# Performance work log

Measured on AMD Instinct MI355X. Metric: run time of the kernel, lower is better.

## Reference

```python
import jax, jax.numpy as jnp
import numpy as np


def ste_sign(x):
    # Forward: q(x) = +1 if x >= 0 else -1.
    # Backward: clipped straight-through estimator (identity on |x| <= 1).
    clipped = jnp.clip(x, -1.0, 1.0)
    binary = jnp.where(x >= 0, 1.0, -1.0).astype(x.dtype)
    return clipped + jax.lax.stop_gradient(binary - clipped)


BATCH = 16384
IN_FEATURES = 4096
UNITS = 512


def setup_inputs() -> dict:
    key = jax.random.key(0)
    kx, kw = jax.random.split(key)
    x = jax.random.normal(kx, (BATCH, IN_FEATURES), dtype=jnp.float32)
    # Latent full-precision kernel (kept in [-1,1]-ish range like a constrained BNN kernel)
    W = jax.random.normal(kw, (IN_FEATURES, UNITS), dtype=jnp.float32) * 0.5
    b = jnp.zeros((UNITS,), dtype=jnp.float32)
    return {"x": x, "W": W, "b": b}


def reference(x, W, b):
    # QuantizedDense: binarize inputs and kernel to +/-1, then standard dense matmul.
    xq = ste_sign(x)                # [B, F]
    Wq = ste_sign(W)                # [F, U]
    return jnp.dot(xq, Wq) + b      # [B, U]
```

## Files before the change

kernel.cpp:

```cpp
#include <hip/hip_runtime.h>
#include <stdint.h>


#define BATCH  16384
#define INF    4096
#define UNITS  512
#define KW     128
#define KW64   64
#define ROWSB  32
#define KC     8
#define NCH    16
#define SWW    12

__global__ __launch_bounds__(256) void pack_w_kernel(const float* __restrict__ W,
                                                     unsigned long long* __restrict__ Wp) {
    int t  = blockIdx.x * 256 + threadIdx.x;
    int u  = t & 511;
    int cj = t >> 9;
    int j  = cj & 3;
    int c  = cj >> 2;
    const float* base = W + (size_t)(c * 256 + j) * UNITS + u;
    unsigned long long m = 0;
    #pragma unroll 16
    for (int i = 0; i < 64; ++i) {
        float v = base[(size_t)(4 * i) * UNITS];
        m |= (unsigned long long)(v < 0.f) << i;
    }
    Wp[(size_t)u * KW64 + cj] = m;
}

__global__ __launch_bounds__(512) void fused_kernel(const float* __restrict__ x,
                                                    const uint32_t* __restrict__ Wp,
                                                    const float* __restrict__ bias,
                                                    float* __restrict__ C) {
    __shared__ __attribute__((aligned(16))) uint32_t sW[2][UNITS][SWW];
    const int t = threadIdx.x;
    const int w = t >> 6;
    const int l = t & 63;
    const int row0 = blockIdx.x * ROWSB;
    const float4* xf4 = reinterpret_cast<const float4*>(x);
    const int wrow = t >> 1;
    const int wcol = (t & 1) * 4;

    uint32_t acc[4][4] = {};
    unsigned long long xb[4][4];

    {
        uint4 wA = *reinterpret_cast<const uint4*>(Wp + (size_t)wrow * KW + wcol);
        uint4 wB = *reinterpret_cast<const uint4*>(Wp + ((size_t)wrow + 256) * KW + wcol);
        #pragma unroll
        for (int i = 0; i < 4; ++i) {
            float4 v = xf4[((size_t)(row0 + w * 4 + i) << 10) + l];
            xb[i][0] = __ballot(v.x < 0.f);
            xb[i][1] = __ballot(v.y < 0.f);
            xb[i][2] = __ballot(v.z < 0.f);
            xb[i][3] = __ballot(v.w < 0.f);
        }
        *reinterpret_cast<uint4*>(&sW[0][wrow][wcol]) = wA;
        *reinterpret_cast<uint4*>(&sW[0][wrow + 256][wcol]) = wB;
        __syncthreads();
    }

    for (int c = 0; c < NCH; ++c) {
        const int cb = c & 1, nb = cb ^ 1;
        const bool pf = (c + 1 < NCH);
        uint4 wA, wB;
        float4 xr[4];

        if (pf) {
            const uint32_t* wsrc = Wp + (c + 1) * KC;
            wA = *reinterpret_cast<const uint4*>(wsrc + (size_t)wrow * KW + wcol);
            wB = *reinterpret_cast<const uint4*>(wsrc + ((size_t)wrow + 256) * KW + wcol);
            #pragma unroll
            for (int i = 0; i < 4; ++i)
                xr[i] = xf4[((size_t)(row0 + w * 4 + i) << 10) + (size_t)(c + 1) * 64 + l];
        }

        #pragma unroll
        for (int j2 = 0; j2 < 4; ++j2) {
            const int u0 = l + 128 * j2;
            uint4 w0a = *reinterpret_cast<const uint4*>(&sW[cb][u0][0]);
            uint4 w0b = *reinterpret_cast<const uint4*>(&sW[cb][u0][4]);
            uint4 w1a = *reinterpret_cast<const uint4*>(&sW[cb][u0 + 64][0]);
            uint4 w1b = *reinterpret_cast<const uint4*>(&sW[cb][u0 + 64][4]);
            #pragma unroll
            for (int i = 0; i < 4; ++i) {
                uint32_t x0 = (uint32_t)xb[i][0], x1 = (uint32_t)(xb[i][0] >> 32);
                uint32_t x2 = (uint32_t)xb[i][1], x3 = (uint32_t)(xb[i][1] >> 32);
                uint32_t x4 = (uint32_t)xb[i][2], x5 = (uint32_t)(xb[i][2] >> 32);
                uint32_t x6 = (uint32_t)xb[i][3], x7 = (uint32_t)(xb[i][3] >> 32);
                uint32_t c0 = __popc(x0 ^ w0a.x) + __popc(x1 ^ w0a.y)
                            + __popc(x2 ^ w0a.z) + __popc(x3 ^ w0a.w)
                            + __popc(x4 ^ w0b.x) + __popc(x5 ^ w0b.y)
                            + __popc(x6 ^ w0b.z) + __popc(x7 ^ w0b.w);
                uint32_t c1 = __popc(x0 ^ w1a.x) + __popc(x1 ^ w1a.y)
                            + __popc(x2 ^ w1a.z) + __popc(x3 ^ w1a.w)
                            + __popc(x4 ^ w1b.x) + __popc(x5 ^ w1b.y)
                            + __popc(x6 ^ w1b.z) + __popc(x7 ^ w1b.w);
                acc[i][j2] += c0 + (c1 << 16);
            }
        }

        if (pf) {
            *reinterpret_cast<uint4*>(&sW[nb][wrow][wcol]) = wA;
            *reinterpret_cast<uint4*>(&sW[nb][wrow + 256][wcol]) = wB;
            #pragma unroll
            for (int i = 0; i < 4; ++i) {
                xb[i][0] = __ballot(xr[i].x < 0.f);
                xb[i][1] = __ballot(xr[i].y < 0.f);
                xb[i][2] = __ballot(xr[i].z < 0.f);
                xb[i][3] = __ballot(xr[i].w < 0.f);
            }
        }
        __syncthreads();
    }

    #pragma unroll
    for (int j2 = 0; j2 < 4; ++j2) {
        const int u0 = l + 128 * j2, u1 = u0 + 64;
        const float bv0 = bias[u0], bv1 = bias[u1];
        #pragma unroll
        for (int i = 0; i < 4; ++i) {
            size_t r = (size_t)(row0 + w * 4 + i) * UNITS;
            uint32_t pk = acc[i][j2];
            C[r + u0] = (float)(INF - 2 * (int)(pk & 0xFFFFu)) + bv0;
            C[r + u1] = (float)(INF - 2 * (int)(pk >> 16)) + bv1;
        }
    }
}

extern "C" void kernel_launch(void* const* d_in, const int* in_sizes, int n_in,
                              void* d_out, int out_size, void* d_ws, size_t ws_size,
                              hipStream_t stream) {
    const float* x = (const float*)d_in[0];
    const float* W = (const float*)d_in[1];
    const float* b = (const float*)d_in[2];
    float* out = (float*)d_out;

    unsigned long long* Wp = (unsigned long long*)d_ws;

    pack_w_kernel<<<32768 / 256, 256, 0, stream>>>(W, Wp);
    fused_kernel<<<BATCH / ROWSB, 512, 0, stream>>>(
        x, (const uint32_t*)Wp, b, out);
}
```

Before: 99.59 us.

## Stream packed weights from global into registers, dropping the shared-memory staging

The packed weight layout is changed so each lane can load uint4 fragments directly from global memory (L2-resident). The fused kernel drops the double-buffered shared-memory tile and the per-chunk __syncthreads, and uses 256-thread blocks where each wave handles 4 rows independently. Weight prefetch is split into two half-chunks that interleave with the popcount compute. This removes LDS traffic and block barriers, but raises register pressure and sends many redundant weight loads through the cache hierarchy.

```diff
diff --git a/kernel.cpp b/kernel.cpp
--- a/kernel.cpp
+++ b/kernel.cpp
@@ -6,14 +6,10 @@
 #define INF    4096
 #define UNITS  512
 #define KW     128
-#define KW64   64
-#define ROWSB  32
-#define KC     8
 #define NCH    16
-#define SWW    12
 
 __global__ __launch_bounds__(256) void pack_w_kernel(const float* __restrict__ W,
-                                                     unsigned long long* __restrict__ Wp) {
+                                                     uint32_t* __restrict__ Wp2) {
     int t  = blockIdx.x * 256 + threadIdx.x;
     int u  = t & 511;
     int cj = t >> 9;
@@ -26,84 +22,89 @@
         float v = base[(size_t)(4 * i) * UNITS];
         m |= (unsigned long long)(v < 0.f) << i;
     }
-    Wp[(size_t)u * KW64 + cj] = m;
+    uint32_t* dst = Wp2 + ((size_t)(c * 2 + (j >> 1)) * 512 + u) * 4 + 2 * (j & 1);
+    *reinterpret_cast<uint2*>(dst) = make_uint2((uint32_t)m, (uint32_t)(m >> 32));
 }
 
-__global__ __launch_bounds__(512) void fused_kernel(const float* __restrict__ x,
-                                                    const uint32_t* __restrict__ Wp,
-                                                    const float* __restrict__ bias,
-                                                    float* __restrict__ C) {
-    __shared__ __attribute__((aligned(16))) uint32_t sW[2][UNITS][SWW];
-    const int t = threadIdx.x;
-    const int w = t >> 6;
-    const int l = t & 63;
-    const int row0 = blockIdx.x * ROWSB;
+__global__ __launch_bounds__(256, 4) void fused_kernel(const float* __restrict__ x,
+                                                       const uint32_t* __restrict__ Wp2,
+                                                       const float* __restrict__ bias,
+                                                       float* __restrict__ C) {
+    const int t  = threadIdx.x;
+    const int l  = t & 63;
+    const int gw = (blockIdx.x * 256 + t) >> 6;
+    const int row0 = gw * 4;
     const float4* xf4 = reinterpret_cast<const float4*>(x);
-    const int wrow = t >> 1;
-    const int wcol = (t & 1) * 4;
+    const uint4*  Wq  = reinterpret_cast<const uint4*>(Wp2);
 
     uint32_t acc[4][4] = {};
     unsigned long long xb[4][4];
+    float4 xr[4];
+    uint4  wvA[8], wvB[8];
 
-    {
-        uint4 wA = *reinterpret_cast<const uint4*>(Wp + (size_t)wrow * KW + wcol);
-        uint4 wB = *reinterpret_cast<const uint4*>(Wp + ((size_t)wrow + 256) * KW + wcol);
-        #pragma unroll
-        for (int i = 0; i < 4; ++i) {
-            float4 v = xf4[((size_t)(row0 + w * 4 + i) << 10) + l];
-            xb[i][0] = __ballot(v.x < 0.f);
-            xb[i][1] = __ballot(v.y < 0.f);
-            xb[i][2] = __ballot(v.z < 0.f);
-            xb[i][3] = __ballot(v.w < 0.f);
-        }
-        *reinterpret_cast<uint4*>(&sW[0][wrow][wcol]) = wA;
-        *reinterpret_cast<uint4*>(&sW[0][wrow + 256][wcol]) = wB;
-        __syncthreads();
+    #pragma unroll
+    for (int i = 0; i < 4; ++i)
+        xr[i] = xf4[((size_t)(row0 + i) << 10) + l];
+    #pragma unroll
+    for (int jj = 0; jj < 8; ++jj)
+        wvA[jj] = Wq[(size_t)(jj * 64 + l)];
+    #pragma unroll
+    for (int jj = 0; jj < 8; ++jj)
+        wvB[jj] = Wq[(size_t)512 + jj * 64 + l];
+    #pragma unroll
+    for (int i = 0; i < 4; ++i) {
+        xb[i][0] = __ballot(xr[i].x < 0.f);
+        xb[i][1] = __ballot(xr[i].y < 0.f);
+        xb[i][2] = __ballot(xr[i].z < 0.f);
+        xb[i][3] = __ballot(xr[i].w < 0.f);
     }
 
+    #pragma unroll 1
     for (int c = 0; c < NCH; ++c) {
-        const int cb = c & 1, nb = cb ^ 1;
         const bool pf = (c + 1 < NCH);
-        uint4 wA, wB;
-        float4 xr[4];
 
         if (pf) {
-            const uint32_t* wsrc = Wp + (c + 1) * KC;
-            wA = *reinterpret_cast<const uint4*>(wsrc + (size_t)wrow * KW + wcol);
-            wB = *reinterpret_cast<const uint4*>(wsrc + ((size_t)wrow + 256) * KW + wcol);
             #pragma unroll
             for (int i = 0; i < 4; ++i)
-                xr[i] = xf4[((size_t)(row0 + w * 4 + i) << 10) + (size_t)(c + 1) * 64 + l];
+                xr[i] = xf4[((size_t)(row0 + i) << 10) + (size_t)(c + 1) * 64 + l];
         }
 
         #pragma unroll
-        for (int j2 = 0; j2 < 4; ++j2) {
-            const int u0 = l + 128 * j2;
-            uint4 w0a = *reinterpret_cast<const uint4*>(&sW[cb][u0][0]);
-            uint4 w0b = *reinterpret_cast<const uint4*>(&sW[cb][u0][4]);
-            uint4 w1a = *reinterpret_cast<const uint4*>(&sW[cb][u0 + 64][0]);
-            uint4 w1b = *reinterpret_cast<const uint4*>(&sW[cb][u0 + 64][4]);
+        for (int i = 0; i < 4; ++i) {
+            uint32_t x0 = (uint32_t)xb[i][0], x1 = (uint32_t)(xb[i][0] >> 32);
+            uint32_t x2 = (uint32_t)xb[i][1], x3 = (uint32_t)(xb[i][1] >> 32);
             #pragma unroll
-            for (int i = 0; i < 4; ++i) {
-                uint32_t x0 = (uint32_t)xb[i][0], x1 = (uint32_t)(xb[i][0] >> 32);
-                uint32_t x2 = (uint32_t)xb[i][1], x3 = (uint32_t)(xb[i][1] >> 32);
-                uint32_t x4 = (uint32_t)xb[i][2], x5 = (uint32_t)(xb[i][2] >> 32);
-                uint32_t x6 = (uint32_t)xb[i][3], x7 = (uint32_t)(xb[i][3] >> 32);
-                uint32_t c0 = __popc(x0 ^ w0a.x) + __popc(x1 ^ w0a.y)
-                            + __popc(x2 ^ w0a.z) + __popc(x3 ^ w0a.w)
-                            + __popc(x4 ^ w0b.x) + __popc(x5 ^ w0b.y)
-                            + __popc(x6 ^ w0b.z) + __popc(x7 ^ w0b.w);
-                uint32_t c1 = __popc(x0 ^ w1a.x) + __popc(x1 ^ w1a.y)
-                            + __popc(x2 ^ w1a.z) + __popc(x3 ^ w1a.w)
-                            + __popc(x4 ^ w1b.x) + __popc(x5 ^ w1b.y)
-                            + __popc(x6 ^ w1b.z) + __popc(x7 ^ w1b.w);
-                acc[i][j2] += c0 + (c1 << 16);
+            for (int jj = 0; jj < 4; ++jj) {
+                uint32_t lo = __popc(x0 ^ wvA[jj].x) + __popc(x1 ^ wvA[jj].y)
+                            + __popc(x2 ^ wvA[jj].z) + __popc(x3 ^ wvA[jj].w);
+                uint32_t hi = __popc(x0 ^ wvA[jj + 4].x) + __popc(x1 ^ wvA[jj + 4].y)
+                            + __popc(x2 ^ wvA[jj + 4].z) + __popc(x3 ^ wvA[jj + 4].w);
+                acc[i][jj] += lo + (hi << 16);
             }
         }
+        if (pf) {
+            #pragma unroll
+            for (int jj = 0; jj < 8; ++jj)
+                wvA[jj] = Wq[(size_t)(c * 2 + 2) * 512 + jj * 64 + l];
+        }
 
+        #pragma unroll
+        for (int i = 0; i < 4; ++i) {
+            uint32_t x4 = (uint32_t)xb[i][2], x5 = (uint32_t)(xb[i][2] >> 32);
+            uint32_t x6 = (uint32_t)xb[i][3], x7 = (uint32_t)(xb[i][3] >> 32);
+            #pragma unroll
+            for (int jj = 0; jj < 4; ++jj) {
+                uint32_t lo = __popc(x4 ^ wvB[jj].x) + __popc(x5 ^ wvB[jj].y)
+                            + __popc(x6 ^ wvB[jj].z) + __popc(x7 ^ wvB[jj].w);
+                uint32_t hi = __popc(x4 ^ wvB[jj + 4].x) + __popc(x5 ^ wvB[jj + 4].y)
+                            + __popc(x6 ^ wvB[jj + 4].z) + __popc(x7 ^ wvB[jj + 4].w);
+                acc[i][jj] += lo + (hi << 16);
+            }
+        }
         if (pf) {
-            *reinterpret_cast<uint4*>(&sW[nb][wrow][wcol]) = wA;
-            *reinterpret_cast<uint4*>(&sW[nb][wrow + 256][wcol]) = wB;
+            #pragma unroll
+            for (int jj = 0; jj < 8; ++jj)
+                wvB[jj] = Wq[(size_t)(c * 2 + 3) * 512 + jj * 64 + l];
             #pragma unroll
             for (int i = 0; i < 4; ++i) {
                 xb[i][0] = __ballot(xr[i].x < 0.f);
@@ -112,19 +113,18 @@
                 xb[i][3] = __ballot(xr[i].w < 0.f);
             }
         }
-        __syncthreads();
     }
 
     #pragma unroll
-    for (int j2 = 0; j2 < 4; ++j2) {
-        const int u0 = l + 128 * j2, u1 = u0 + 64;
-        const float bv0 = bias[u0], bv1 = bias[u1];
+    for (int jj = 0; jj < 4; ++jj) {
+        const int u0 = l + 64 * jj, u1 = u0 + 256;
+        const float b0 = bias[u0], b1 = bias[u1];
         #pragma unroll
         for (int i = 0; i < 4; ++i) {
-            size_t r = (size_t)(row0 + w * 4 + i) * UNITS;
-            uint32_t pk = acc[i][j2];
-            C[r + u0] = (float)(INF - 2 * (int)(pk & 0xFFFFu)) + bv0;
-            C[r + u1] = (float)(INF - 2 * (int)(pk >> 16)) + bv1;
+            size_t r = (size_t)(row0 + i) * UNITS;
+            uint32_t pk = acc[i][jj];
+            C[r + u0] = (float)(INF - 2 * (int)(pk & 0xFFFFu)) + b0;
+            C[r + u1] = (float)(INF - 2 * (int)(pk >> 16)) + b1;
         }
     }
 }
@@ -137,9 +137,8 @@
     const float* b = (const float*)d_in[2];
     float* out = (float*)d_out;
 
-    unsigned long long* Wp = (unsigned long long*)d_ws;
+    uint32_t* Wp2 = (uint32_t*)d_ws;
 
-    pack_w_kernel<<<32768 / 256, 256, 0, stream>>>(W, Wp);
-    fused_kernel<<<BATCH / ROWSB, 512, 0, stream>>>(
-        x, (const uint32_t*)Wp, b, out);
+    pack_w_kernel<<<32768 / 256, 256, 0, stream>>>(W, Wp2);
+    fused_kernel<<<BATCH / 16, 256, 0, stream>>>(x, Wp2, b, out);
 }
```

Result: slower. 393.9 us (+295.5%).
